# Kernel tuning notes

Hardware: AMD Instinct MI355X
Metric: run time of the kernel (lower is better)

The kernel has to match this reference:

```python
import jax, jax.numpy as jnp
import numpy as np

T = 8192   # sequence length (sent_len)
D = 512    # word_emb_dim
H = 2048   # enc_lstm_dim
S = 512    # number of segments (len(action_pos))
EPS = 1e-4 # additive constant in the original _masked_softmax denominator


def setup_inputs() -> dict:
    key = jax.random.key(0)
    ks = jax.random.split(key, 16)
    s = 0.02  # small init scale keeps exp() stable
    seg_len = T // S
    action_pos = (jnp.arange(1, S + 1, dtype=jnp.int32) * seg_len - 1)  # last = T-1
    action = jnp.zeros((T,), jnp.int32).at[action_pos].set(1)
    return {
        "sent": jax.random.normal(ks[0], (T, D), jnp.float32),
        "Wi1": jax.random.normal(ks[1], (3 * H, D), jnp.float32) * s,
        "Wh1": jax.random.normal(ks[2], (3 * H, H), jnp.float32) * s,
        "bi1": jax.random.normal(ks[3], (3 * H,), jnp.float32) * s,
        "bh1": jax.random.normal(ks[4], (3 * H,), jnp.float32) * s,
        "Wi2": jax.random.normal(ks[5], (3 * H, H), jnp.float32) * s,
        "Wh2": jax.random.normal(ks[6], (3 * H, H), jnp.float32) * s,
        "bi2": jax.random.normal(ks[7], (3 * H,), jnp.float32) * s,
        "bh2": jax.random.normal(ks[8], (3 * H,), jnp.float32) * s,
        "Wl": jax.random.normal(ks[9], (H, H), jnp.float32) * s,
        "bl": jax.random.normal(ks[10], (H,), jnp.float32) * s,
        "wa": jax.random.normal(ks[11], (H,), jnp.float32) * s,
        "Wl2": jax.random.normal(ks[12], (H, H), jnp.float32) * s,
        "bl2": jax.random.normal(ks[13], (H,), jnp.float32) * s,
        "wa2": jax.random.normal(ks[14], (H,), jnp.float32) * s,
        "action": action,
        "action_pos": action_pos,
    }


def _gru_scan(xs, reset, Wi, Wh, bi, bh):
    """GRU over leading axis; hidden state zeroed after steps where reset==1.
    xs: (N, in), reset: (N,) int. Returns outputs (N, H)."""
    gi_all = xs @ Wi.T + bi  # (N, 3H) precompute input gates as one GEMM

    def step(h, inp):
        gi, a = inp
        gh = Wh @ h + bh
        r = jax.nn.sigmoid(gi[:H] + gh[:H])
        z = jax.nn.sigmoid(gi[H:2 * H] + gh[H:2 * H])
        n = jnp.tanh(gi[2 * H:] + r * gh[2 * H:])
        hn = (1.0 - z) * n + z * h
        h_next = jnp.where(a == 1, jnp.zeros_like(hn), hn)
        return h_next, hn

    h0 = jnp.zeros((H,), xs.dtype)
    _, outs = jax.lax.scan(step, h0, (gi_all, reset))
    return outs


def _degenerate_softmax(a):
    # Original sums exp over a size-1 axis: w = exp(a) / (exp(a) + 1e-4)
    e = jnp.exp(a)
    return e / (e + EPS)


def reference(sent, Wi1, Wh1, bi1, bh1, Wi2, Wh2, bi2, bh2,
              Wl, bl, wa, Wl2, bl2, wa2, action, action_pos):
    # lower GRU with per-step state reset
    outs = _gru_scan(sent, action, Wi1, Wh1, bi1, bh1)          # (T, H)
    emb_h = jnp.tanh(outs @ Wl.T + bl)                           # (T, H)
    w = _degenerate_softmax(emb_h @ wa)                          # (T,)
    weighted = w[:, None] * emb_h                                # (T, H)
    # segment i covers tokens (action_pos[i-1], action_pos[i]]
    seg_id = jnp.searchsorted(action_pos, jnp.arange(T), side='left')
    seg = jax.ops.segment_max(weighted, seg_id, num_segments=S)  # (S, H)
    # upper GRU over segment embeddings (no resets, zero init)
    outs2 = _gru_scan(seg, jnp.zeros((S,), jnp.int32), Wi2, Wh2, bi2, bh2)
    e2 = jnp.tanh(outs2 @ Wl2.T + bl2)                           # (S, H)
    w2 = _degenerate_softmax(e2 @ wa2)                           # (S,)
    emb = jnp.max(w2[:, None] * e2, axis=0, keepdims=True)       # (1, H)
    return emb
```

## Files before the change

kernel.cpp:

```cpp
#include <hip/hip_runtime.h>
#include <stdint.h>

typedef unsigned short u16;
typedef unsigned int u32;
typedef unsigned long long u64;
typedef __attribute__((ext_vector_type(4))) float f32x4;
typedef __attribute__((ext_vector_type(8))) short bf16x8;
typedef __attribute__((ext_vector_type(4))) u32 u32x4;

constexpr int kT = 8192;
constexpr int kD = 512;
constexpr int kH = 2048;
constexpr int kH3 = 6144;
constexpr int kS = 512;
constexpr int kSeg = 16;
constexpr int kNWG2 = 256;
constexpr int kREP = 4;

__device__ __forceinline__ float bf2f(u16 u) {
  union { float f; u32 u; } v; v.u = ((u32)u) << 16; return v.f;
}
__device__ __forceinline__ u16 f2bf(float f) {
  union { float f; u32 u; } v; v.f = f;
  u32 lsb = (v.u >> 16) & 1u;
  v.u += 0x7fffu + lsb;
  return (u16)(v.u >> 16);
}
__device__ __forceinline__ float bflo(u32 x) {
  union { float f; u32 u; } v; v.u = x << 16; return v.f;
}
__device__ __forceinline__ float bfhi(u32 x) {
  union { float f; u32 u; } v; v.u = x & 0xffff0000u; return v.f;
}
__device__ __forceinline__ float sigm(float x) { return 1.f / (1.f + expf(-x)); }

__device__ __forceinline__ void g2l16(const u16* g, u16* l) {
  __builtin_amdgcn_global_load_lds(
      (const __attribute__((address_space(1))) u32*)g,
      (__attribute__((address_space(3))) u32*)l, 16, 0, 0);
}

__device__ __forceinline__ u32x4 bypass_load16(const u32* p) {
  u32x4 v;
  asm volatile("global_load_dwordx4 %0, %1, off sc0 sc1\n\ts_waitcnt vmcnt(0)"
               : "=&v"(v) : "v"(p) : "memory");
  return v;
}
__device__ __forceinline__ void bypass_store16(u32* p, u32x4 v) {
  asm volatile("global_store_dwordx4 %0, %1, off sc0 sc1" :: "v"(p), "v"(v) : "memory");
}

__global__ void cvt_bf16(const float* __restrict__ in, u16* __restrict__ out, int n4) {
  int i = blockIdx.x * blockDim.x + threadIdx.x;
  if (i >= n4) return;
  const float4 v = *(const float4*)(in + (size_t)i * 4);
  uint2 o;
  o.x = (u32)f2bf(v.x) | ((u32)f2bf(v.y) << 16);
  o.y = (u32)f2bf(v.z) | ((u32)f2bf(v.w) << 16);
  *(uint2*)(out + (size_t)i * 4) = o;
}

template<int EPI>
__global__ __launch_bounds__(256)
void gemm_bt(const u16* __restrict__ A, int lda,
             const u16* __restrict__ B, int ldb,
             u16* __restrict__ Obf, const float* __restrict__ bias,
             int M, int N, int K)
{
  __shared__ u16 ls[4 * 16384];
  const int tid = threadIdx.x;
  const int w = tid >> 6, lane = tid & 63;
  const int wr = w >> 1, wc = w & 1;
  const int arow0 = blockIdx.y * 128;
  const int brow0 = blockIdx.x * 128;
  const int srow = w * 32 + (lane >> 3);
  const int scol = (lane & 7) * 8;
  const u16* gA = A + (size_t)(arow0 + srow) * lda + scol;
  const u16* gB = B + (size_t)(brow0 + srow) * ldb + scol;
  const int sb = w * 32 * 64;

  f32x4 acc[4][4];
#pragma unroll
  for (int m = 0; m < 4; ++m)
#pragma unroll
    for (int n = 0; n < 4; ++n) acc[m][n] = (f32x4)0.f;

  const int fr = lane & 15;
  const int kq = lane >> 4;
  const int nk = K >> 6;

  auto stage = [&](int buf, int kt) {
    u16* la = &ls[buf * 16384 + sb];
    u16* lb = &ls[buf * 16384 + 8192 + sb];
#pragma unroll
    for (int i = 0; i < 4; ++i) g2l16(gA + (size_t)i * 8 * lda + kt, la + i * 8 * 64);
#pragma unroll
    for (int i = 0; i < 4; ++i) g2l16(gB + (size_t)i * 8 * ldb + kt, lb + i * 8 * 64);
  };

  stage(0, 0);
  if (nk > 1) stage(1, 64);
  if (nk > 2) stage(2, 128);

  for (int i = 0; i < nk; ++i) {
    if (i + 2 < nk) asm volatile("s_waitcnt vmcnt(16)" ::: "memory");
    else            asm volatile("s_waitcnt vmcnt(0)" ::: "memory");
    __builtin_amdgcn_s_barrier();
    __builtin_amdgcn_sched_barrier(0);
    if (i + 3 < nk) stage((i + 3) & 3, (i + 3) * 64);
    const u16* lsA = &ls[(i & 3) * 16384];
    const u16* lsB = lsA + 8192;
#pragma unroll
    for (int kk = 0; kk < 2; ++kk) {
      bf16x8 af[4], bq[4];
#pragma unroll
      for (int m = 0; m < 4; ++m)
        af[m] = *(const bf16x8*)&lsA[(wr * 64 + m * 16 + fr) * 64 + kk * 32 + kq * 8];
#pragma unroll
      for (int n = 0; n < 4; ++n)
        bq[n] = *(const bf16x8*)&lsB[(wc * 64 + n * 16 + fr) * 64 + kk * 32 + kq * 8];
#pragma unroll
      for (int m = 0; m < 4; ++m)
#pragma unroll
        for (int n = 0; n < 4; ++n)
          acc[m][n] = __builtin_amdgcn_mfma_f32_16x16x32_bf16(af[m], bq[n], acc[m][n], 0, 0, 0);
    }
  }

#pragma unroll
  for (int m = 0; m < 4; ++m) {
#pragma unroll
    for (int n = 0; n < 4; ++n) {
      const int row0 = arow0 + wr * 64 + m * 16 + kq * 4;
      const int col = brow0 + wc * 64 + n * 16 + fr;
      if (EPI == 1) {
#pragma unroll
        for (int i = 0; i < 4; ++i)
          Obf[(size_t)(row0 + i) * N + col] = f2bf(acc[m][n][i]);
      } else {
        const float bv = bias[col];
#pragma unroll
        for (int i = 0; i < 4; ++i)
          Obf[(size_t)(row0 + i) * N + col] = f2bf(tanhf(acc[m][n][i] + bv));
      }
    }
  }
}

__global__ __launch_bounds__(256) void gru1_gates(
    const u16* __restrict__ gi, const u16* __restrict__ gh,
    const float* __restrict__ bi, const float* __restrict__ bh,
    u16* __restrict__ h_bf, u16* __restrict__ outs_bf, int t)
{
  const int idx = blockIdx.x * 256 + threadIdx.x;
  const int seg = idx >> 10, jp = idx & 1023;
  const u32* gi32 = (const u32*)gi;
  const u32* gh32 = (const u32*)gh;
  const int base = seg * 3072;
  const u32 gir = gi32[base + jp],        ghr = gh32[base + jp];
  const u32 giz = gi32[base + 1024 + jp], ghz = gh32[base + 1024 + jp];
  const u32 gin = gi32[base + 2048 + jp], ghn = gh32[base + 2048 + jp];
  const float2 bir = *(const float2*)&bi[2 * jp];
  const float2 biz = *(const float2*)&bi[kH + 2 * jp];
  const float2 bin = *(const float2*)&bi[2 * kH + 2 * jp];
  const float2 bhr = *(const float2*)&bh[2 * jp];
  const float2 bhz = *(const float2*)&bh[kH + 2 * jp];
  const float2 bhn = *(const float2*)&bh[2 * kH + 2 * jp];
  const u32 hp = ((const u32*)h_bf)[seg * 1024 + jp];
  float hn[2];
#pragma unroll
  for (int e = 0; e < 2; ++e) {
    const float gr = e ? bfhi(gir) : bflo(gir), hr = e ? bfhi(ghr) : bflo(ghr);
    const float gz = e ? bfhi(giz) : bflo(giz), hz = e ? bfhi(ghz) : bflo(ghz);
    const float gn = e ? bfhi(gin) : bflo(gin), hh = e ? bfhi(ghn) : bflo(ghn);
    const float r = sigm(gr + (e ? bir.y : bir.x) + hr + (e ? bhr.y : bhr.x));
    const float z = sigm(gz + (e ? biz.y : biz.x) + hz + (e ? bhz.y : bhz.x));
    const float n = tanhf(gn + (e ? bin.y : bin.x) + r * (hh + (e ? bhn.y : bhn.x)));
    const float hprev = e ? bfhi(hp) : bflo(hp);
    hn[e] = (1.f - z) * n + z * hprev;
  }
  const u32 packed = (u32)f2bf(hn[0]) | ((u32)f2bf(hn[1]) << 16);
  ((u32*)h_bf)[seg * 1024 + jp] = packed;
  ((u32*)outs_bf)[(size_t)(seg * kSeg + t) * 1024 + jp] = packed;
}

__global__ __launch_bounds__(256) void seg_weight_max(
    const u16* __restrict__ embh, const float* __restrict__ wa,
    u16* __restrict__ seg_bf)
{
  __shared__ float wrow[16];
  const int s = blockIdx.x, tid = threadIdx.x;
  const int w = tid >> 6, lane = tid & 63;
#pragma unroll
  for (int rr = 0; rr < 4; ++rr) {
    const int r = w * 4 + rr;
    const u16* row = embh + ((size_t)s * kSeg + r) * kH;
    float p = 0.f;
#pragma unroll
    for (int k = 0; k < 32; ++k) {
      const int c = lane + 64 * k;
      p += bf2f(row[c]) * wa[c];
    }
#pragma unroll
    for (int off = 32; off; off >>= 1) p += __shfl_down(p, off, 64);
    if (lane == 0) { const float e = expf(p); wrow[r] = e / (e + 1e-4f); }
  }
  __syncthreads();
#pragma unroll
  for (int i = 0; i < 8; ++i) {
    const int c = tid + 256 * i;
    float m = -1e30f;
#pragma unroll
    for (int r = 0; r < 16; ++r)
      m = fmaxf(m, wrow[r] * bf2f(embh[((size_t)s * kSeg + r) * kH + c]));
    seg_bf[(size_t)s * kH + c] = f2bf(m);
  }
}

__global__ __launch_bounds__(512)
void gru2_persistent(const u16* __restrict__ Wh2bf, const u16* __restrict__ gi2b,
                     const float* __restrict__ bi2, const float* __restrict__ bh2,
                     u32* __restrict__ hx,
                     u16* __restrict__ outs2)
{
  __shared__ u16 wl[24 * kH];
  __shared__ u32 hlb[1024];
  __shared__ float gil_all[512 * 24];
  __shared__ float rowsum[24];
  __shared__ alignas(16) u16 hnl[8];
  const int wg = blockIdx.x, tid = threadIdx.x;
  const int g0 = wg * 8;
  const int rep = wg & (kREP - 1);
  uint4* wl4 = (uint4*)wl;
  for (int i = tid; i < 24 * 256; i += 512) {
    const int lr = i >> 8, q = i & 255;
    const int grow = (lr >> 3) * kH + g0 + (lr & 7);
    wl4[i] = ((const uint4*)Wh2bf)[(size_t)grow * 256 + q];
  }
  for (int i = tid; i < 512 * 24; i += 512) {
    const int t = i / 24, idx = i - t * 24;
    gil_all[i] = bf2f(gi2b[(size_t)t * kH3 + (idx >> 3) * kH + g0 + (idx & 7)]);
  }
  float bir = 0, biz = 0, bin = 0, bhr = 0, bhz = 0, bhn = 0;
  if (tid < 8) {
    const int jj = g0 + tid;
    bir = bi2[jj]; biz = bi2[kH + jj]; bin = bi2[2 * kH + jj];
    bhr = bh2[jj]; bhz = bh2[kH + jj]; bhn = bh2[2 * kH + jj];
  }
  const int w = tid >> 6, lane = tid & 63;
  const uint4* hl4 = (const uint4*)hlb;

  for (int t = 0; t < 512; ++t) {
    const u32 want = (u32)t & 0xffffu;
    const u32* p = hx + ((size_t)(t & 1) * kREP + rep) * 2048 + 4 * tid;
    u32x4 v;
    for (;;) {
      v = bypass_load16(p);
      const u32 bad = ((v.x ^ want) | (v.y ^ want) | (v.z ^ want) | (v.w ^ want)) & 0xffffu;
      if (!__any((int)bad)) break;
      __builtin_amdgcn_s_sleep(1);
    }
    hlb[2 * tid]     = (v.x >> 16) | (v.y & 0xffff0000u);
    hlb[2 * tid + 1] = (v.z >> 16) | (v.w & 0xffff0000u);
    __syncthreads();
#pragma unroll
    for (int rr = 0; rr < 3; ++rr) {
      const int lr = w * 3 + rr;
      float p2 = 0.f;
#pragma unroll
      for (int k = 0; k < 4; ++k) {
        const int q = lane + 64 * k;
        const uint4 wv = wl4[lr * 256 + q];
        const uint4 hv = hl4[q];
        p2 += bflo(wv.x) * bflo(hv.x) + bfhi(wv.x) * bfhi(hv.x);
        p2 += bflo(wv.y) * bflo(hv.y) + bfhi(wv.y) * bfhi(hv.y);
        p2 += bflo(wv.z) * bflo(hv.z) + bfhi(wv.z) * bfhi(hv.z);
        p2 += bflo(wv.w) * bflo(hv.w) + bfhi(wv.w) * bfhi(hv.w);
      }
#pragma unroll
      for (int off = 32; off; off >>= 1) p2 += __shfl_down(p2, off, 64);
      if (lane == 0) rowsum[lr] = p2;
    }
    __syncthreads();
    if (tid < 8) {
      const float r = sigm(gil_all[t * 24 + tid] + bir + rowsum[tid] + bhr);
      const float z = sigm(gil_all[t * 24 + 8 + tid] + biz + rowsum[8 + tid] + bhz);
      const float n = tanhf(gil_all[t * 24 + 16 + tid] + bin +
                            r * (rowsum[16 + tid] + bhn));
      const u32 hw = hlb[(g0 + tid) >> 1];
      const float hprev = (tid & 1) ? bfhi(hw) : bflo(hw);
      hnl[tid] = f2bf((1.f - z) * n + z * hprev);
    }
    __syncthreads();
    if (tid < 2 * kREP) {
      const int orep = tid >> 1, half = tid & 1;
      const u16* h4 = hnl + half * 4;
      const u32 tagv = (u32)(t + 1) & 0xffffu;
      u32x4 m;
      m.x = ((u32)h4[0] << 16) | tagv;
      m.y = ((u32)h4[1] << 16) | tagv;
      m.z = ((u32)h4[2] << 16) | tagv;
      m.w = ((u32)h4[3] << 16) | tagv;
      u32* q = hx + ((size_t)((t + 1) & 1) * kREP + orep) * 2048 + wg * 8 + half * 4;
      bypass_store16(q, m);
    }
    if (tid == 0)
      *(uint4*)&outs2[(size_t)t * kH + g0] = *(const uint4*)hnl;
  }
}

__global__ void calc_w2(const u16* __restrict__ e2, const float* __restrict__ wa2,
                        float* __restrict__ w2) {
  const int s = blockIdx.x, lane = threadIdx.x;
  float p = 0.f;
#pragma unroll
  for (int k = 0; k < 32; ++k) {
    const int c = lane + 64 * k;
    p += bf2f(e2[(size_t)s * kH + c]) * wa2[c];
  }
#pragma unroll
  for (int off = 32; off; off >>= 1) p += __shfl_down(p, off, 64);
  if (lane == 0) { const float e = expf(p); w2[s] = e / (e + 1e-4f); }
}

__global__ void final_max(const u16* __restrict__ e2, const float* __restrict__ w2,
                          float* __restrict__ out) {
  const int j = blockIdx.x * blockDim.x + threadIdx.x;
  float m = -1e30f;
  for (int s = 0; s < 512; ++s)
    m = fmaxf(m, w2[s] * bf2f(e2[(size_t)s * kH + j]));
  out[j] = m;
}

extern "C" void kernel_launch(void* const* d_in, const int* in_sizes, int n_in,
                              void* d_out, int out_size, void* d_ws, size_t ws_size,
                              hipStream_t stream)
{
  (void)in_sizes; (void)n_in; (void)out_size; (void)ws_size;
  const float* sent = (const float*)d_in[0];
  const float* Wi1f = (const float*)d_in[1];
  const float* Wh1f = (const float*)d_in[2];
  const float* bi1  = (const float*)d_in[3];
  const float* bh1  = (const float*)d_in[4];
  const float* Wi2f = (const float*)d_in[5];
  const float* Wh2f = (const float*)d_in[6];
  const float* bi2  = (const float*)d_in[7];
  const float* bh2  = (const float*)d_in[8];
  const float* Wlf  = (const float*)d_in[9];
  const float* bl   = (const float*)d_in[10];
  const float* wa   = (const float*)d_in[11];
  const float* Wl2f = (const float*)d_in[12];
  const float* bl2  = (const float*)d_in[13];
  const float* wa2  = (const float*)d_in[14];
  float* out = (float*)d_out;

  char* base = (char*)d_ws;
  size_t off = 0;
  auto alloc = [&](size_t b) { char* p = base + off; off += (b + 255) & ~(size_t)255; return p; };
  u16* sent_bf = (u16*)alloc((size_t)kT * kD * 2);
  u16* Wi1b    = (u16*)alloc((size_t)kH3 * kD * 2);
  u16* Wh1b    = (u16*)alloc((size_t)kH3 * kH * 2);
  u16* Wi2b    = (u16*)alloc((size_t)kH3 * kH * 2);
  u16* Wh2b    = (u16*)alloc((size_t)kH3 * kH * 2);
  u16* Wlb     = (u16*)alloc((size_t)kH * kH * 2);
  u16* Wl2b    = (u16*)alloc((size_t)kH * kH * 2);
  u16* gi_buf  = (u16*)alloc((size_t)kS * kH3 * 2);
  u16* gh_buf  = (u16*)alloc((size_t)kS * kH3 * 2);
  u16* h1b     = (u16*)alloc((size_t)kS * kH * 2);
  u16* outs_bf = (u16*)alloc((size_t)kT * kH * 2);
  u16* seg_bf  = (u16*)alloc((size_t)kS * kH * 2);
  u32* hx      = (u32*)alloc((size_t)2 * kREP * 2048 * 4);
  u16* outs2   = (u16*)alloc((size_t)kS * kH * 2);
  u16* e2b     = (u16*)alloc((size_t)kS * kH * 2);
  float* w2    = (float*)alloc(kS * 4);
  u16* embh = sent_bf;
  u16* gi2b = gi_buf;

  (void)hipMemsetAsync(h1b, 0, (size_t)kS * kH * 2, stream);
  (void)hipMemsetAsync(hx, 0, (size_t)2 * kREP * 2048 * 4, stream);

  auto cvt = [&](const float* src, u16* dst, int n) {
    const int n4 = n / 4;
    cvt_bf16<<<dim3((n4 + 255) / 256), dim3(256), 0, stream>>>(src, dst, n4);
  };
  cvt(sent, sent_bf, kT * kD);
  cvt(Wi1f, Wi1b, kH3 * kD);
  cvt(Wh1f, Wh1b, kH3 * kH);
  cvt(Wi2f, Wi2b, kH3 * kH);
  cvt(Wlf, Wlb, kH * kH);
  cvt(Wl2f, Wl2b, kH * kH);
  cvt(Wh2f, Wh2b, kH3 * kH);

  for (int t = 0; t < kSeg; ++t) {
    gemm_bt<1><<<dim3(kH3 / 128, kS / 128), dim3(256), 0, stream>>>(
        h1b, kH, Wh1b, kH, gh_buf, nullptr, kS, kH3, kH);
    gemm_bt<1><<<dim3(kH3 / 128, kS / 128), dim3(256), 0, stream>>>(
        sent_bf + t * kD, kSeg * kD, Wi1b, kD, gi_buf, nullptr, kS, kH3, kD);
    gru1_gates<<<dim3(kS * kH / 512), dim3(256), 0, stream>>>(
        gi_buf, gh_buf, bi1, bh1, h1b, outs_bf, t);
  }
  gemm_bt<2><<<dim3(kH / 128, kT / 128), dim3(256), 0, stream>>>(
      outs_bf, kH, Wlb, kH, embh, bl, kT, kH, kH);
  seg_weight_max<<<dim3(kS), dim3(256), 0, stream>>>(embh, wa, seg_bf);
  gemm_bt<1><<<dim3(kH3 / 128, kS / 128), dim3(256), 0, stream>>>(
      seg_bf, kH, Wi2b, kH, gi2b, nullptr, kS, kH3, kH);
  gru2_persistent<<<dim3(kNWG2), dim3(512), 0, stream>>>(
      Wh2b, gi2b, bi2, bh2, hx, outs2);
  gemm_bt<2><<<dim3(kH / 128, kS / 128), dim3(256), 0, stream>>>(
      outs2, kH, Wl2b, kH, e2b, bl2, kS, kH, kH);
  calc_w2<<<dim3(kS), dim3(64), 0, stream>>>(e2b, wa2, w2);
  final_max<<<dim3(kH / 256), dim3(256), 0, stream>>>(e2b, w2, out);
}
```

Before: 2.979 ms.

## Precompute all lower-GRU input gates in one large GEMM and tweak spin-wait

When the workspace is large enough, the input-gate projection for all 8192 tokens is computed by one big GEMM before the time loop, replacing 16 small per-step GEMMs. The gate kernel now reads from this buffer with a segment stride. The aim is better GPU utilisation and fewer launches, at the cost of a 100MB buffer and extra memory traffic. The upper GRU spin-wait also now re-polls only lanes that still see stale data, with a longer sleep between polls.

```diff
diff --git a/kernel.cpp b/kernel.cpp
--- a/kernel.cpp
+++ b/kernel.cpp
@@ -148,18 +148,18 @@
 }
 
 __global__ __launch_bounds__(256) void gru1_gates(
-    const u16* __restrict__ gi, const u16* __restrict__ gh,
+    const u32* __restrict__ gi32, int segStride, const u16* __restrict__ gh,
     const float* __restrict__ bi, const float* __restrict__ bh,
     u16* __restrict__ h_bf, u16* __restrict__ outs_bf, int t)
 {
   const int idx = blockIdx.x * 256 + threadIdx.x;
   const int seg = idx >> 10, jp = idx & 1023;
-  const u32* gi32 = (const u32*)gi;
   const u32* gh32 = (const u32*)gh;
+  const int gbase = seg * segStride;
   const int base = seg * 3072;
-  const u32 gir = gi32[base + jp],        ghr = gh32[base + jp];
-  const u32 giz = gi32[base + 1024 + jp], ghz = gh32[base + 1024 + jp];
-  const u32 gin = gi32[base + 2048 + jp], ghn = gh32[base + 2048 + jp];
+  const u32 gir = gi32[gbase + jp],        ghr = gh32[base + jp];
+  const u32 giz = gi32[gbase + 1024 + jp], ghz = gh32[base + 1024 + jp];
+  const u32 gin = gi32[gbase + 2048 + jp], ghn = gh32[base + 2048 + jp];
   const float2 bir = *(const float2*)&bi[2 * jp];
   const float2 biz = *(const float2*)&bi[kH + 2 * jp];
   const float2 bin = *(const float2*)&bi[2 * kH + 2 * jp];
@@ -253,12 +253,14 @@
   for (int t = 0; t < 512; ++t) {
     const u32 want = (u32)t & 0xffffu;
     const u32* p = hx + ((size_t)(t & 1) * kREP + rep) * 2048 + 4 * tid;
-    u32x4 v;
+    u32x4 v = bypass_load16(p);
     for (;;) {
-      v = bypass_load16(p);
       const u32 bad = ((v.x ^ want) | (v.y ^ want) | (v.z ^ want) | (v.w ^ want)) & 0xffffu;
       if (!__any((int)bad)) break;
-      __builtin_amdgcn_s_sleep(1);
+      if (bad) {
+        __builtin_amdgcn_s_sleep(2);
+        v = bypass_load16(p);
+      }
     }
     hlb[2 * tid]     = (v.x >> 16) | (v.y & 0xffff0000u);
     hlb[2 * tid + 1] = (v.z >> 16) | (v.w & 0xffff0000u);
@@ -336,7 +338,7 @@
                               void* d_out, int out_size, void* d_ws, size_t ws_size,
                               hipStream_t stream)
 {
-  (void)in_sizes; (void)n_in; (void)out_size; (void)ws_size;
+  (void)in_sizes; (void)n_in; (void)out_size;
   const float* sent = (const float*)d_in[0];
   const float* Wi1f = (const float*)d_in[1];
   const float* Wh1f = (const float*)d_in[2];
@@ -373,6 +375,10 @@
   u16* outs2   = (u16*)alloc((size_t)kS * kH * 2);
   u16* e2b     = (u16*)alloc((size_t)kS * kH * 2);
   float* w2    = (float*)alloc(kS * 4);
+  const size_t off_before_gi = off;
+  u16* gi_all  = (u16*)alloc((size_t)kT * kH3 * 2);
+  const bool fused_gi = (off <= ws_size);
+  if (!fused_gi) off = off_before_gi;
   u16* embh = sent_bf;
   u16* gi2b = gi_buf;
 
@@ -391,13 +397,26 @@
   cvt(Wl2f, Wl2b, kH * kH);
   cvt(Wh2f, Wh2b, kH3 * kH);
 
+  if (fused_gi) {
+    gemm_bt<1><<<dim3(kH3 / 128, kT / 128), dim3(256), 0, stream>>>(
+        sent_bf, kD, Wi1b, kD, gi_all, nullptr, kT, kH3, kD);
+  }
   for (int t = 0; t < kSeg; ++t) {
     gemm_bt<1><<<dim3(kH3 / 128, kS / 128), dim3(256), 0, stream>>>(
         h1b, kH, Wh1b, kH, gh_buf, nullptr, kS, kH3, kH);
-    gemm_bt<1><<<dim3(kH3 / 128, kS / 128), dim3(256), 0, stream>>>(
-        sent_bf + t * kD, kSeg * kD, Wi1b, kD, gi_buf, nullptr, kS, kH3, kD);
+    const u32* gi32;
+    int segStride;
+    if (fused_gi) {
+      gi32 = (const u32*)gi_all + (size_t)t * 3072;
+      segStride = kSeg * 3072;
+    } else {
+      gemm_bt<1><<<dim3(kH3 / 128, kS / 128), dim3(256), 0, stream>>>(
+          sent_bf + t * kD, kSeg * kD, Wi1b, kD, gi_buf, nullptr, kS, kH3, kD);
+      gi32 = (const u32*)gi_buf;
+      segStride = 3072;
+    }
     gru1_gates<<<dim3(kS * kH / 512), dim3(256), 0, stream>>>(
-        gi_buf, gh_buf, bi1, bh1, h1b, outs_bf, t);
+        gi32, segStride, gh_buf, bi1, bh1, h1b, outs_bf, t);
   }
   gemm_bt<2><<<dim3(kH / 128, kT / 128), dim3(256), 0, stream>>>(
       outs_bf, kH, Wlb, kH, embh, bl, kT, kH, kH);
```

New measurement: 2.972 ms. No clear change (-0.2%).
